# Performance work log

Measured on AMD Instinct MI355X. Metric: run time of the kernel, lower is better.

Reference implementation:

```python
import jax, jax.numpy as jnp
import numpy as np

B, N, D = 2, 2048, 1024
H = 16
DH = D // H
SCALE = 1.0 / np.sqrt(D).astype(np.float32)  # faithful: module uses 1/sqrt(d_out), not head_dim


def setup_inputs() -> dict:
    key = jax.random.key(0)
    ks = jax.random.split(key, 5)
    s = 0.02
    return {
        "x": jax.random.normal(ks[0], (B, N, D), dtype=jnp.float32),
        "Wq": jax.random.normal(ks[1], (D, D), dtype=jnp.float32) * s,
        "Wk": jax.random.normal(ks[2], (D, D), dtype=jnp.float32) * s,
        "Wv": jax.random.normal(ks[3], (D, D), dtype=jnp.float32) * s,
        "Wo": jax.random.normal(ks[4], (D, D), dtype=jnp.float32) * s,
        "bo": jnp.zeros((D,), dtype=jnp.float32),
    }


def reference(x, Wq, Wk, Wv, Wo, bo):
    b, n, _ = x.shape
    # qkv projections (no bias), split heads: [b, H, n, DH]
    q = (x @ Wq).reshape(b, n, H, DH).transpose(0, 2, 1, 3)
    k = (x @ Wk).reshape(b, n, H, DH).transpose(0, 2, 1, 3)
    v = (x @ Wv).reshape(b, n, H, DH).transpose(0, 2, 1, 3)
    # full N x N scores (the module materializes this)
    scores = jnp.einsum("bhqd,bhkd->bhqk", q, k)
    causal = jnp.triu(jnp.ones((n, n), dtype=bool), k=1)  # True above diagonal -> masked
    scores = jnp.where(causal[None, None], -jnp.inf, scores)
    # faithful order: mask first, then scale, then softmax (-inf * scale stays -inf)
    attn = jax.nn.softmax(scores * SCALE, axis=-1)
    ctx = jnp.einsum("bhqk,bhkd->bhqd", attn, v)
    ctx = ctx.transpose(0, 2, 1, 3).reshape(b, n, D)
    return ctx @ Wo + bo
```

## Files before the change

### kernel.cpp

```cpp
#include <hip/hip_runtime.h>
#include <stdint.h>

#define H 16
#define DH 64
#define BATCH 2
#define NSEQ 2048
#define DMODEL 1024
#define QSZ (BATCH*H*NSEQ*DH)
#define ATT_CS 0.04508422017f

typedef __attribute__((ext_vector_type(8))) short short8;
typedef __attribute__((ext_vector_type(4))) short shortx4;
typedef __attribute__((ext_vector_type(4))) float floatx4;

__device__ __forceinline__ short f2bf(float f) {
  union { float f; unsigned u; } c; c.f = f;
  unsigned u = c.u;
  unsigned r = (u + 0x7FFFu + ((u >> 16) & 1u)) >> 16;
  return (short)r;
}

__device__ __forceinline__ unsigned pk2bf(float a, float b) {
  union { float f; unsigned u; } ca, cb; ca.f = a; cb.f = b;
  return __builtin_amdgcn_perm(cb.u + 0x8000u, ca.u + 0x8000u, 0x07060302u);
}

__device__ __forceinline__ void gld_lds16(const short* g, short* l) {
  __builtin_amdgcn_global_load_lds((const __attribute__((address_space(1))) unsigned int*)g,
                                   (__attribute__((address_space(3))) unsigned int*)l,
                                   16, 0, 0);
}

__global__ __launch_bounds__(256) void prep_kernel(const float* __restrict__ x,
                                                   const float* __restrict__ Wq,
                                                   const float* __restrict__ Wk,
                                                   const float* __restrict__ Wv,
                                                   const float* __restrict__ Wo,
                                                   short* __restrict__ xb,
                                                   short* __restrict__ wqkvt,
                                                   short* __restrict__ wot) {
  __shared__ short tile[32][33];
  int bid = blockIdx.x;
  if (bid < 4096) {
    int i = bid * 256 + threadIdx.x;
    float4 v = ((const float4*)x)[i];
    short4 o;
    o.x = f2bf(v.x); o.y = f2bf(v.y); o.z = f2bf(v.z); o.w = f2bf(v.w);
    ((short4*)xb)[i] = o;
  } else {
    int t = bid - 4096;
    int widx = t >> 10, rem = t & 1023;
    int bx = rem & 31, by = rem >> 5;
    const float* W = (widx == 0) ? Wq : (widx == 1) ? Wk : (widx == 2) ? Wv : Wo;
    short* dst = (widx < 3) ? (wqkvt + (size_t)widx * 1048576) : wot;
    int k0 = bx * 32, n0 = by * 32;
    int tx = threadIdx.x & 31, ty = threadIdx.x >> 5;
#pragma unroll
    for (int i = 0; i < 4; i++) {
      int k = k0 + ty + i * 8;
      tile[tx][ty + i * 8] = f2bf(W[(size_t)k * DMODEL + n0 + tx]);
    }
    __syncthreads();
#pragma unroll
    for (int i = 0; i < 4; i++) {
      int n = n0 + ty + i * 8;
      dst[(size_t)n * DMODEL + k0 + tx] = tile[ty + i * 8][tx];
    }
  }
}

template <int MODE>
__global__ __launch_bounds__(256) void gemm_bt(const short* __restrict__ A,
                                               const short* __restrict__ Bt,
                                               short* __restrict__ outb,
                                               float* __restrict__ outf,
                                               const float* __restrict__ bias,
                                               int K, int nbn) {
  __shared__ __align__(16) short As[2][4096];
  __shared__ __align__(16) short Bs[2][4096];
  int tid = threadIdx.x;
  int lane = tid & 63;
  int w = tid >> 6;
  int wm = w >> 1, wn = w & 1;
  int m16 = lane & 15, quad = lane >> 4;
  int bm = blockIdx.x / nbn, bn = blockIdx.x % nbn;

  floatx4 acc[4][4];
#pragma unroll
  for (int i = 0; i < 4; i++)
#pragma unroll
    for (int j = 0; j < 4; j++) acc[i][j] = (floatx4){0.f, 0.f, 0.f, 0.f};

  const short* Ablk = A + (size_t)bm * 128 * K;
  const short* Bblk = Bt + (size_t)bn * 128 * K;

  auto stage = [&](int k0, int b) {
#pragma unroll
    for (int t = 0; t < 2; t++) {
      int e = w * 1024 + t * 512 + lane * 8;
      int row = e >> 5, col = e & 31;
      gld_lds16(Ablk + (size_t)row * K + k0 + col, &As[b][w * 1024 + t * 512]);
      gld_lds16(Bblk + (size_t)row * K + k0 + col, &Bs[b][w * 1024 + t * 512]);
    }
  };

  stage(0, 0);
  for (int k0 = 0; k0 < K; k0 += 32) {
    int b = (k0 >> 5) & 1;
    __syncthreads();
    if (k0 + 32 < K) stage(k0 + 32, b ^ 1);
    short8 af[4], bfr[4];
#pragma unroll
    for (int i = 0; i < 4; i++)
      af[i] = *(const short8*)&As[b][(wm * 64 + i * 16 + m16) * 32 + quad * 8];
#pragma unroll
    for (int j = 0; j < 4; j++)
      bfr[j] = *(const short8*)&Bs[b][(wn * 64 + j * 16 + m16) * 32 + quad * 8];
#pragma unroll
    for (int i = 0; i < 4; i++)
#pragma unroll
      for (int j = 0; j < 4; j++)
        acc[i][j] = __builtin_amdgcn_mfma_f32_16x16x32_bf16(af[i], bfr[j], acc[i][j], 0, 0, 0);
  }

#pragma unroll
  for (int i = 0; i < 4; i++) {
    int mrow_base = bm * 128 + wm * 64 + i * 16 + quad * 4;
#pragma unroll
    for (int j = 0; j < 4; j++) {
      int ncol = bn * 128 + wn * 64 + j * 16 + m16;
      if (MODE == 0) {
        int which = ncol >> 10;
        int c = ncol & 1023;
        int h = c >> 6, dh = c & 63;
        int b = mrow_base >> 11, ns0 = mrow_base & 2047;
        if (which == 2) {
          shortx4 pk;
#pragma unroll
          for (int r = 0; r < 4; r++) pk[r] = f2bf(acc[i][j][r]);
          *(shortx4*)&outb[2 * (size_t)QSZ + (((size_t)(b * H + h) * DH + dh) * NSEQ) + ns0] = pk;
        } else {
          float sc = (which == 0) ? ATT_CS : 1.0f;
#pragma unroll
          for (int r = 0; r < 4; r++)
            outb[(size_t)which * QSZ + (((size_t)(b * H + h) * NSEQ + ns0 + r) * DH) + dh] =
                f2bf(acc[i][j][r] * sc);
        }
      } else {
#pragma unroll
        for (int r = 0; r < 4; r++)
          outf[(size_t)(mrow_base + r) * DMODEL + ncol] = acc[i][j][r] + bias[ncol];
      }
    }
  }
}

__global__ __launch_bounds__(256) void attn_kernel(const short* __restrict__ Qw,
                                                   const short* __restrict__ Kw,
                                                   const short* __restrict__ VtG,
                                                   short* __restrict__ ctx) {
  __shared__ __align__(16) short Ks[4096];
  __shared__ __align__(16) short Vt[4096];
  __shared__ __align__(16) short Ps[2][4][16 * 72];
  int bh = blockIdx.y;
  int tid = threadIdx.x, lane = tid & 63, w = tid >> 6;
  int m16 = lane & 15, quad = lane >> 4;
  int sw = m16 & 7;
  const size_t base = (size_t)bh * NSEQ * DH;
  const short* Kg0 = Kw + base;
  const short* Vg0 = VtG + base;
  short* PwA = &Ps[0][w][0];
  short* PwB = &Ps[1][w][0];

  int qbA = blockIdx.x;
  int qbB = 31 - qbA;
  int q0A = qbA * 64 + w * 16;
  int q0B = qbB * 64 + w * 16;

  short8 qfA[2], qfB[2];
#pragma unroll
  for (int kk = 0; kk < 2; kk++) {
    qfA[kk] = *(const short8*)(Qw + base + (size_t)(q0A + m16) * DH + kk * 32 + quad * 8);
    qfB[kk] = *(const short8*)(Qw + base + (size_t)(q0B + m16) * DH + kk * 32 + quad * 8);
  }

  float mA = -__builtin_inff(), lA = 0.f, mB = -__builtin_inff(), lB = 0.f;
  floatx4 oA[4], oB[4];
#pragma unroll
  for (int d = 0; d < 4; d++) { oA[d] = (floatx4){0.f,0.f,0.f,0.f}; oB[d] = (floatx4){0.f,0.f,0.f,0.f}; }

  short8 kf[4][2], vf[4][2];

  auto stage = [&](int kc) {
#pragma unroll
    for (int t = 0; t < 2; t++) {
      int e = w * 1024 + t * 512 + lane * 8;
      int r = e >> 6;
      int g = ((e >> 3) & 7) ^ (r & 7);
      gld_lds16(Kg0 + (size_t)(kc * 64 + r) * DH + g * 8, &Ks[w * 1024 + t * 512]);
      gld_lds16(Vg0 + (size_t)r * NSEQ + kc * 64 + g * 8, &Vt[w * 1024 + t * 512]);
    }
  };

  auto tile_qk = [&](bool diag, int kc, int q0, const short8* qf,
                     float& m, float& l, float& alpha, short* Pw) {
    floatx4 st[4];
#pragma unroll
    for (int nj = 0; nj < 4; nj++) {
      floatx4 s = (floatx4){0.f, 0.f, 0.f, 0.f};
      s = __builtin_amdgcn_mfma_f32_16x16x32_bf16(kf[nj][0], qf[0], s, 0, 0, 0);
      s = __builtin_amdgcn_mfma_f32_16x16x32_bf16(kf[nj][1], qf[1], s, 0, 0, 0);
      st[nj] = s;
    }
    int qrow = q0 + m16;
    float tv[16];
    float mloc = -__builtin_inff();
#pragma unroll
    for (int nj = 0; nj < 4; nj++)
#pragma unroll
      for (int r = 0; r < 4; r++) {
        float v = st[nj][r];
        if (diag) {
          int key = kc * 64 + nj * 16 + quad * 4 + r;
          if (key > qrow) v = -__builtin_inff();
        }
        tv[nj * 4 + r] = v;
        mloc = fmaxf(mloc, v);
      }
    float mx = fmaxf(mloc, __shfl_xor(mloc, 16, 64));
    mx = fmaxf(mx, __shfl_xor(mx, 32, 64));
    float mnew = fmaxf(m, mx);
    alpha = __builtin_amdgcn_exp2f(m - mnew);
    float sum = 0.f;
#pragma unroll
    for (int nj = 0; nj < 4; nj++) {
      float p0 = __builtin_amdgcn_exp2f(tv[nj * 4 + 0] - mnew);
      float p1 = __builtin_amdgcn_exp2f(tv[nj * 4 + 1] - mnew);
      float p2 = __builtin_amdgcn_exp2f(tv[nj * 4 + 2] - mnew);
      float p3 = __builtin_amdgcn_exp2f(tv[nj * 4 + 3] - mnew);
      sum += (p0 + p1) + (p2 + p3);
      uint2 pk;
      pk.x = pk2bf(p0, p1);
      pk.y = pk2bf(p2, p3);
      *(uint2*)&Pw[m16 * 72 + nj * 16 + quad * 4] = pk;
    }
    sum += __shfl_xor(sum, 16, 64);
    sum += __shfl_xor(sum, 32, 64);
    l = l * alpha + sum;
    m = mnew;
  };

  auto tile_pv = [&](float alpha, floatx4* o, const short* Pw) {
    short8 pf[2];
    pf[0] = *(const short8*)&Pw[m16 * 72 + quad * 8];
    pf[1] = *(const short8*)&Pw[m16 * 72 + 32 + quad * 8];
#pragma unroll
    for (int d = 0; d < 4; d++) {
      o[d] *= alpha;
#pragma unroll
      for (int kj = 0; kj < 2; kj++)
        o[d] = __builtin_amdgcn_mfma_f32_16x16x32_bf16(vf[d][kj], pf[kj], o[d], 0, 0, 0);
    }
  };

  for (int kc = 0; kc <= qbB; ++kc) {
    __syncthreads();
    stage(kc);
    __syncthreads();
#pragma unroll
    for (int nj = 0; nj < 4; nj++) {
      kf[nj][0] = *(const short8*)&Ks[(nj * 16 + m16) * 64 + ((quad ^ sw) * 8)];
      kf[nj][1] = *(const short8*)&Ks[(nj * 16 + m16) * 64 + (((4 + quad) ^ sw) * 8)];
    }
#pragma unroll
    for (int d = 0; d < 4; d++) {
      vf[d][0] = *(const short8*)&Vt[(d * 16 + m16) * 64 + ((quad ^ sw) * 8)];
      vf[d][1] = *(const short8*)&Vt[(d * 16 + m16) * 64 + (((4 + quad) ^ sw) * 8)];
    }
    if (kc <= qbA) {
      float aA, aB;
      tile_qk(kc == qbA, kc, q0A, qfA, mA, lA, aA, PwA);
      tile_qk(false,     kc, q0B, qfB, mB, lB, aB, PwB);
      tile_pv(aA, oA, PwA);
      tile_pv(aB, oB, PwB);
    } else {
      float aB;
      tile_qk(kc == qbB, kc, q0B, qfB, mB, lB, aB, PwB);
      tile_pv(aB, oB, PwB);
    }
  }

  int b = bh >> 4, h = bh & 15;
#pragma unroll
  for (int s = 0; s < 2; s++) {
    int q0 = s ? q0B : q0A;
    float inv = 1.f / (s ? lB : lA);
    floatx4* o = s ? oB : oA;
    size_t rowbase = ((size_t)(b * NSEQ + q0 + m16)) * DMODEL + h * DH;
#pragma unroll
    for (int d = 0; d < 4; d++) {
      shortx4 pk;
#pragma unroll
      for (int r = 0; r < 4; r++) pk[r] = f2bf(o[d][r] * inv);
      *(shortx4*)&ctx[rowbase + d * 16 + quad * 4] = pk;
    }
  }
}

extern "C" void kernel_launch(void* const* d_in, const int* in_sizes, int n_in,
                              void* d_out, int out_size, void* d_ws, size_t ws_size,
                              hipStream_t stream) {
  const float* x  = (const float*)d_in[0];
  const float* Wq = (const float*)d_in[1];
  const float* Wk = (const float*)d_in[2];
  const float* Wv = (const float*)d_in[3];
  const float* Wo = (const float*)d_in[4];
  const float* bo = (const float*)d_in[5];
  float* out = (float*)d_out;

  char* ws = (char*)d_ws;
  short* xb    = (short*)(ws);
  short* wqkvt = (short*)(ws + (8ull << 20));
  short* wot   = (short*)(ws + (14ull << 20));
  short* qkvws = (short*)(ws + (16ull << 20));
  short* ctx   = (short*)(ws + (40ull << 20));

  prep_kernel<<<8192, 256, 0, stream>>>(x, Wq, Wk, Wv, Wo, xb, wqkvt, wot);

  gemm_bt<0><<<32 * 24, 256, 0, stream>>>(xb, wqkvt, qkvws, nullptr, nullptr, 1024, 24);

  short* qws = qkvws;
  short* kws = qkvws + QSZ;
  short* vtg = qkvws + 2 * QSZ;
  dim3 ag(16, BATCH * H);
  attn_kernel<<<ag, 256, 0, stream>>>(qws, kws, vtg, ctx);

  gemm_bt<1><<<32 * 8, 256, 0, stream>>>(ctx, wot, nullptr, out, bo, 1024, 8);
}
```

Before: 201.7 us.

## Halve attention block size and narrow output GEMM tile to raise block counts

The attention kernel drops from 4 to 2 waves per block and covers 32 query rows per block instead of 64, launching 32 column blocks per head instead of 16. Each wave now stages twice as much of the K/V tiles. The output projection GEMM becomes templated on N-tile width and uses a 128x64 tile, doubling its grid from 256 to 512 blocks. Both changes aim to fill more of the GPU's compute units, at the cost of more redundant K/V and A-tile loads and less reuse per block.

```diff
diff --git a/kernel.cpp b/kernel.cpp
--- a/kernel.cpp
+++ b/kernel.cpp
@@ -69,15 +69,16 @@
   }
 }
 
-template <int MODE>
+template <int MODE, int NT>
 __global__ __launch_bounds__(256) void gemm_bt(const short* __restrict__ A,
                                                const short* __restrict__ Bt,
                                                short* __restrict__ outb,
                                                float* __restrict__ outf,
                                                const float* __restrict__ bias,
                                                int K, int nbn) {
+  constexpr int JF = NT / 32;
   __shared__ __align__(16) short As[2][4096];
-  __shared__ __align__(16) short Bs[2][4096];
+  __shared__ __align__(16) short Bs[2][NT * 32];
   int tid = threadIdx.x;
   int lane = tid & 63;
   int w = tid >> 6;
@@ -85,14 +86,14 @@
   int m16 = lane & 15, quad = lane >> 4;
   int bm = blockIdx.x / nbn, bn = blockIdx.x % nbn;
 
-  floatx4 acc[4][4];
+  floatx4 acc[4][JF];
 #pragma unroll
   for (int i = 0; i < 4; i++)
 #pragma unroll
-    for (int j = 0; j < 4; j++) acc[i][j] = (floatx4){0.f, 0.f, 0.f, 0.f};
+    for (int j = 0; j < JF; j++) acc[i][j] = (floatx4){0.f, 0.f, 0.f, 0.f};
 
   const short* Ablk = A + (size_t)bm * 128 * K;
-  const short* Bblk = Bt + (size_t)bn * 128 * K;
+  const short* Bblk = Bt + (size_t)bn * NT * K;
 
   auto stage = [&](int k0, int b) {
 #pragma unroll
@@ -100,7 +101,18 @@
       int e = w * 1024 + t * 512 + lane * 8;
       int row = e >> 5, col = e & 31;
       gld_lds16(Ablk + (size_t)row * K + k0 + col, &As[b][w * 1024 + t * 512]);
-      gld_lds16(Bblk + (size_t)row * K + k0 + col, &Bs[b][w * 1024 + t * 512]);
+    }
+    if constexpr (NT == 128) {
+#pragma unroll
+      for (int t = 0; t < 2; t++) {
+        int e = w * 1024 + t * 512 + lane * 8;
+        int row = e >> 5, col = e & 31;
+        gld_lds16(Bblk + (size_t)row * K + k0 + col, &Bs[b][w * 1024 + t * 512]);
+      }
+    } else {
+      int e = w * 512 + lane * 8;
+      int row = e >> 5, col = e & 31;
+      gld_lds16(Bblk + (size_t)row * K + k0 + col, &Bs[b][w * 512]);
     }
   };
 
@@ -109,17 +121,17 @@
     int b = (k0 >> 5) & 1;
     __syncthreads();
     if (k0 + 32 < K) stage(k0 + 32, b ^ 1);
-    short8 af[4], bfr[4];
+    short8 af[4], bfr[JF];
 #pragma unroll
     for (int i = 0; i < 4; i++)
       af[i] = *(const short8*)&As[b][(wm * 64 + i * 16 + m16) * 32 + quad * 8];
 #pragma unroll
-    for (int j = 0; j < 4; j++)
-      bfr[j] = *(const short8*)&Bs[b][(wn * 64 + j * 16 + m16) * 32 + quad * 8];
+    for (int j = 0; j < JF; j++)
+      bfr[j] = *(const short8*)&Bs[b][(wn * (NT / 2) + j * 16 + m16) * 32 + quad * 8];
 #pragma unroll
     for (int i = 0; i < 4; i++)
 #pragma unroll
-      for (int j = 0; j < 4; j++)
+      for (int j = 0; j < JF; j++)
         acc[i][j] = __builtin_amdgcn_mfma_f32_16x16x32_bf16(af[i], bfr[j], acc[i][j], 0, 0, 0);
   }
 
@@ -127,8 +139,8 @@
   for (int i = 0; i < 4; i++) {
     int mrow_base = bm * 128 + wm * 64 + i * 16 + quad * 4;
 #pragma unroll
-    for (int j = 0; j < 4; j++) {
-      int ncol = bn * 128 + wn * 64 + j * 16 + m16;
+    for (int j = 0; j < JF; j++) {
+      int ncol = bn * NT + wn * (NT / 2) + j * 16 + m16;
       if (MODE == 0) {
         int which = ncol >> 10;
         int c = ncol & 1023;
@@ -155,13 +167,13 @@
   }
 }
 
-__global__ __launch_bounds__(256) void attn_kernel(const short* __restrict__ Qw,
+__global__ __launch_bounds__(128) void attn_kernel(const short* __restrict__ Qw,
                                                    const short* __restrict__ Kw,
                                                    const short* __restrict__ VtG,
                                                    short* __restrict__ ctx) {
   __shared__ __align__(16) short Ks[4096];
   __shared__ __align__(16) short Vt[4096];
-  __shared__ __align__(16) short Ps[2][4][16 * 72];
+  __shared__ __align__(16) short Ps[2][2][16 * 72];
   int bh = blockIdx.y;
   int tid = threadIdx.x, lane = tid & 63, w = tid >> 6;
   int m16 = lane & 15, quad = lane >> 4;
@@ -172,10 +184,11 @@
   short* PwA = &Ps[0][w][0];
   short* PwB = &Ps[1][w][0];
 
-  int qbA = blockIdx.x;
-  int qbB = 31 - qbA;
-  int q0A = qbA * 64 + w * 16;
-  int q0B = qbB * 64 + w * 16;
+  int bx = blockIdx.x;
+  int qbA = bx >> 1;
+  int qbB = (63 - bx) >> 1;
+  int q0A = bx * 32 + w * 16;
+  int q0B = (63 - bx) * 32 + w * 16;
 
   short8 qfA[2], qfB[2];
 #pragma unroll
@@ -193,12 +206,12 @@
 
   auto stage = [&](int kc) {
 #pragma unroll
-    for (int t = 0; t < 2; t++) {
-      int e = w * 1024 + t * 512 + lane * 8;
+    for (int t = 0; t < 4; t++) {
+      int e = w * 2048 + t * 512 + lane * 8;
       int r = e >> 6;
       int g = ((e >> 3) & 7) ^ (r & 7);
-      gld_lds16(Kg0 + (size_t)(kc * 64 + r) * DH + g * 8, &Ks[w * 1024 + t * 512]);
-      gld_lds16(Vg0 + (size_t)r * NSEQ + kc * 64 + g * 8, &Vt[w * 1024 + t * 512]);
+      gld_lds16(Kg0 + (size_t)(kc * 64 + r) * DH + g * 8, &Ks[w * 2048 + t * 512]);
+      gld_lds16(Vg0 + (size_t)r * NSEQ + kc * 64 + g * 8, &Vt[w * 2048 + t * 512]);
     }
   };
 
@@ -327,13 +340,13 @@
 
   prep_kernel<<<8192, 256, 0, stream>>>(x, Wq, Wk, Wv, Wo, xb, wqkvt, wot);
 
-  gemm_bt<0><<<32 * 24, 256, 0, stream>>>(xb, wqkvt, qkvws, nullptr, nullptr, 1024, 24);
+  gemm_bt<0, 128><<<32 * 24, 256, 0, stream>>>(xb, wqkvt, qkvws, nullptr, nullptr, 1024, 24);
 
   short* qws = qkvws;
   short* kws = qkvws + QSZ;
   short* vtg = qkvws + 2 * QSZ;
-  dim3 ag(16, BATCH * H);
-  attn_kernel<<<ag, 256, 0, stream>>>(qws, kws, vtg, ctx);
-
-  gemm_bt<1><<<32 * 8, 256, 0, stream>>>(ctx, wot, nullptr, out, bo, 1024, 8);
-}
+  dim3 ag(32, BATCH * H);
+  attn_kernel<<<ag, 128, 0, stream>>>(qws, kws, vtg, ctx);
+
+  gemm_bt<1, 64><<<32 * 16, 256, 0, stream>>>(ctx, wot, nullptr, out, bo, 1024, 16);
+}
```

Result: slower. 229.5 us (+13.8%).
